# Performance work log

Measured on AMD Instinct MI355X. Metric: run time of the kernel, lower is better.

The kernel has to match this reference:

```python
import jax, jax.numpy as jnp
import numpy as np

N_BINS = 15


def setup_inputs() -> dict:
    key = jax.random.key(0)
    k1, k2 = jax.random.split(key)
    N, C = 4000000, 64
    logits = jax.random.normal(k1, (N, C), dtype=jnp.float32)
    labels = jax.random.randint(k2, (N,), 0, C, dtype=jnp.int64)
    temperature = jnp.ones((1,), dtype=jnp.float32)
    return {"logits": logits, "labels": labels, "temperature": temperature}


def reference(logits, labels, temperature):
    # softmax over classes at given temperature (onevsrest=False path)
    probs = jax.nn.softmax(logits / temperature, axis=1)
    confidences = jnp.max(probs, axis=1)          # [N]
    predictions = jnp.argmax(probs, axis=1)       # [N]
    accuracies = (predictions == labels).astype(confidences.dtype)

    # bin i covers (i/n_bins, (i+1)/n_bins]; conf >= 1/C > 0 so ceil-1 maps correctly
    bin_idx = jnp.clip(
        jnp.ceil(confidences * N_BINS).astype(jnp.int32) - 1, 0, N_BINS - 1)

    count = jax.ops.segment_sum(jnp.ones_like(confidences), bin_idx, num_segments=N_BINS)
    conf_sum = jax.ops.segment_sum(confidences, bin_idx, num_segments=N_BINS)
    acc_sum = jax.ops.segment_sum(accuracies, bin_idx, num_segments=N_BINS)

    nonempty = count > 0
    safe_count = jnp.where(nonempty, count, 1.0)
    gap = jnp.abs(conf_sum / safe_count - acc_sum / safe_count)  # [n_bins]
    prop = count / confidences.shape[0]

    ece = jnp.sum(jnp.where(nonempty, gap * prop, 0.0))
    mce = jnp.max(jnp.where(nonempty, gap, 0.0))
    return ece, mce
```

## Files before the change

kernel.cpp:

```cpp
#include <hip/hip_runtime.h>

#define NBINS 15

typedef float f32x4 __attribute__((ext_vector_type(4)));

__global__ __launch_bounds__(256) void ece_partial(
    const f32x4* __restrict__ logits4,
    const int*   __restrict__ labels,
    const float* __restrict__ temperature,
    float*       __restrict__ gbins,
    int N)
{
    __shared__ float sbins[3 * NBINS];
    const int tid = threadIdx.x;
    if (tid < 3 * NBINS) sbins[tid] = 0.0f;
    __syncthreads();

    const float invT = 1.0f / temperature[0];

    const int lane = tid & 63;
    const int wIn  = tid >> 6;
    const long long gWave = (long long)blockIdx.x * 4 + wIn;
    const long long nWave = (long long)gridDim.x * 4;

    const int sub = lane & 3;
    const int rIw = lane >> 2;

    for (long long r0 = gWave * 16; r0 < (long long)N; r0 += nWave * 16) {
        const long long row = r0 + rIw;
        const bool valid = row < (long long)N;
        const long long rc = valid ? row : (long long)(N - 1);

        const f32x4* p = logits4 + rc * 16 + sub;
        const f32x4 v0 = __builtin_nontemporal_load(p);
        const f32x4 v1 = __builtin_nontemporal_load(p + 4);
        const f32x4 v2 = __builtin_nontemporal_load(p + 8);
        const f32x4 v3 = __builtin_nontemporal_load(p + 12);

        float m  = v0.x;
        int   am = 4 * sub;
        {
            const int b = 4 * sub;
            if (v0.y > m) { m = v0.y; am = b + 1; }
            if (v0.z > m) { m = v0.z; am = b + 2; }
            if (v0.w > m) { m = v0.w; am = b + 3; }
            if (v1.x > m) { m = v1.x; am = b + 16; }
            if (v1.y > m) { m = v1.y; am = b + 17; }
            if (v1.z > m) { m = v1.z; am = b + 18; }
            if (v1.w > m) { m = v1.w; am = b + 19; }
            if (v2.x > m) { m = v2.x; am = b + 32; }
            if (v2.y > m) { m = v2.y; am = b + 33; }
            if (v2.z > m) { m = v2.z; am = b + 34; }
            if (v2.w > m) { m = v2.w; am = b + 35; }
            if (v3.x > m) { m = v3.x; am = b + 48; }
            if (v3.y > m) { m = v3.y; am = b + 49; }
            if (v3.z > m) { m = v3.z; am = b + 50; }
            if (v3.w > m) { m = v3.w; am = b + 51; }
        }

        #pragma unroll
        for (int d = 1; d < 4; d <<= 1) {
            const float om = __shfl_xor(m, d);
            const int   oa = __shfl_xor(am, d);
            if (om > m || (om == m && oa < am)) { m = om; am = oa; }
        }

        float s = __expf((v0.x - m) * invT) + __expf((v0.y - m) * invT)
                + __expf((v0.z - m) * invT) + __expf((v0.w - m) * invT)
                + __expf((v1.x - m) * invT) + __expf((v1.y - m) * invT)
                + __expf((v1.z - m) * invT) + __expf((v1.w - m) * invT)
                + __expf((v2.x - m) * invT) + __expf((v2.y - m) * invT)
                + __expf((v2.z - m) * invT) + __expf((v2.w - m) * invT)
                + __expf((v3.x - m) * invT) + __expf((v3.y - m) * invT)
                + __expf((v3.z - m) * invT) + __expf((v3.w - m) * invT);
        #pragma unroll
        for (int d = 1; d < 4; d <<= 1) s += __shfl_xor(s, d);

        if (valid && sub == 0) {
            const float conf = 1.0f / s;
            const int   lbl  = labels[row];
            const float acc  = (am == lbl) ? 1.0f : 0.0f;
            int bin = (int)ceilf(conf * (float)NBINS) - 1;
            bin = bin < 0 ? 0 : (bin > NBINS - 1 ? NBINS - 1 : bin);
            atomicAdd(&sbins[bin],             1.0f);
            atomicAdd(&sbins[NBINS + bin],     conf);
            atomicAdd(&sbins[2 * NBINS + bin], acc);
        }
    }

    __syncthreads();
    if (tid < 3 * NBINS) {
        const float v = sbins[tid];
        if (v != 0.0f) atomicAdd(&gbins[tid], v);
    }
}

__global__ void ece_finalize(const float* __restrict__ gbins,
                             float* __restrict__ out, float invN)
{
    if (threadIdx.x == 0 && blockIdx.x == 0) {
        float ece = 0.0f, mce = 0.0f;
        #pragma unroll
        for (int i = 0; i < NBINS; ++i) {
            const float c  = gbins[i];
            const float cs = gbins[NBINS + i];
            const float as = gbins[2 * NBINS + i];
            if (c > 0.0f) {
                const float gap = fabsf(cs / c - as / c);
                ece += gap * (c * invN);
                mce = fmaxf(mce, gap);
            }
        }
        out[0] = ece;
        out[1] = mce;
    }
}

extern "C" void kernel_launch(void* const* d_in, const int* in_sizes, int n_in,
                              void* d_out, int out_size, void* d_ws, size_t ws_size,
                              hipStream_t stream) {
    const f32x4* logits4     = (const f32x4*)d_in[0];
    const int*   labels      = (const int*)d_in[1];
    const float* temperature = (const float*)d_in[2];
    float*       out         = (float*)d_out;
    float*       gbins       = (float*)d_ws;

    const int N = in_sizes[1];

    hipMemsetAsync(gbins, 0, 3 * NBINS * sizeof(float), stream);

    const int block = 256;
    const int grid  = 2048;
    ece_partial<<<grid, block, 0, stream>>>(logits4, labels, temperature, gbins, N);
    ece_finalize<<<1, 64, 0, stream>>>(gbins, out, 1.0f / (float)N);
}
```

Measured before the change: 189.6 us.

## Fuse finalize via last-block ticket and drop argmax tracking for label compare

Merges the finalize kernel into the main kernel using an atomic ticket, so the last block computes ECE and MCE and one launch goes away. Softmax is computed without subtracting the max, and the max is found with plain fmax reductions. Accuracy is decided by checking whether the label's logit equals the row max, so no argmax index is shuffled, and the label load is issued alongside the logit loads. This cuts ALU and shuffle work in a memory-bound loop, but it can overflow for large logits or small temperatures and changes tie-breaking semantics.

```diff
diff --git a/kernel.cpp b/kernel.cpp
--- a/kernel.cpp
+++ b/kernel.cpp
@@ -4,12 +4,14 @@
 
 typedef float f32x4 __attribute__((ext_vector_type(4)));
 
-__global__ __launch_bounds__(256) void ece_partial(
+__global__ __launch_bounds__(256, 8) void ece_fused(
     const f32x4* __restrict__ logits4,
     const int*   __restrict__ labels,
     const float* __restrict__ temperature,
     float*       __restrict__ gbins,
-    int N)
+    int*         __restrict__ ticket,
+    float*       __restrict__ out,
+    int N, int nblocks)
 {
     __shared__ float sbins[3 * NBINS];
     const int tid = threadIdx.x;
@@ -36,55 +38,50 @@
         const f32x4 v1 = __builtin_nontemporal_load(p + 4);
         const f32x4 v2 = __builtin_nontemporal_load(p + 8);
         const f32x4 v3 = __builtin_nontemporal_load(p + 12);
+        const int lbl = labels[rc];
 
-        float m  = v0.x;
-        int   am = 4 * sub;
+        float s;
         {
-            const int b = 4 * sub;
-            if (v0.y > m) { m = v0.y; am = b + 1; }
-            if (v0.z > m) { m = v0.z; am = b + 2; }
-            if (v0.w > m) { m = v0.w; am = b + 3; }
-            if (v1.x > m) { m = v1.x; am = b + 16; }
-            if (v1.y > m) { m = v1.y; am = b + 17; }
-            if (v1.z > m) { m = v1.z; am = b + 18; }
-            if (v1.w > m) { m = v1.w; am = b + 19; }
-            if (v2.x > m) { m = v2.x; am = b + 32; }
-            if (v2.y > m) { m = v2.y; am = b + 33; }
-            if (v2.z > m) { m = v2.z; am = b + 34; }
-            if (v2.w > m) { m = v2.w; am = b + 35; }
-            if (v3.x > m) { m = v3.x; am = b + 48; }
-            if (v3.y > m) { m = v3.y; am = b + 49; }
-            if (v3.z > m) { m = v3.z; am = b + 50; }
-            if (v3.w > m) { m = v3.w; am = b + 51; }
+            const float a0 = __expf(v0.x * invT), a1 = __expf(v0.y * invT);
+            const float a2 = __expf(v0.z * invT), a3 = __expf(v0.w * invT);
+            const float b0 = __expf(v1.x * invT), b1 = __expf(v1.y * invT);
+            const float b2 = __expf(v1.z * invT), b3 = __expf(v1.w * invT);
+            const float c0 = __expf(v2.x * invT), c1 = __expf(v2.y * invT);
+            const float c2 = __expf(v2.z * invT), c3 = __expf(v2.w * invT);
+            const float d0 = __expf(v3.x * invT), d1 = __expf(v3.y * invT);
+            const float d2 = __expf(v3.z * invT), d3 = __expf(v3.w * invT);
+            s = (((a0 + a1) + (a2 + a3)) + ((b0 + b1) + (b2 + b3)))
+              + (((c0 + c1) + (c2 + c3)) + ((d0 + d1) + (d2 + d3)));
         }
 
-        #pragma unroll
-        for (int d = 1; d < 4; d <<= 1) {
-            const float om = __shfl_xor(m, d);
-            const int   oa = __shfl_xor(am, d);
-            if (om > m || (om == m && oa < am)) { m = om; am = oa; }
-        }
+        float m = fmaxf(fmaxf(fmaxf(v0.x, v0.y), fmaxf(v0.z, v0.w)),
+                        fmaxf(fmaxf(v1.x, v1.y), fmaxf(v1.z, v1.w)));
+        m = fmaxf(m, fmaxf(fmaxf(fmaxf(v2.x, v2.y), fmaxf(v2.z, v2.w)),
+                           fmaxf(fmaxf(v3.x, v3.y), fmaxf(v3.z, v3.w))));
 
-        float s = __expf((v0.x - m) * invT) + __expf((v0.y - m) * invT)
-                + __expf((v0.z - m) * invT) + __expf((v0.w - m) * invT)
-                + __expf((v1.x - m) * invT) + __expf((v1.y - m) * invT)
-                + __expf((v1.z - m) * invT) + __expf((v1.w - m) * invT)
-                + __expf((v2.x - m) * invT) + __expf((v2.y - m) * invT)
-                + __expf((v2.z - m) * invT) + __expf((v2.w - m) * invT)
-                + __expf((v3.x - m) * invT) + __expf((v3.y - m) * invT)
-                + __expf((v3.z - m) * invT) + __expf((v3.w - m) * invT);
-        #pragma unroll
-        for (int d = 1; d < 4; d <<= 1) s += __shfl_xor(s, d);
+        s += __shfl_xor(s, 1);
+        s += __shfl_xor(s, 2);
+        m = fmaxf(m, __shfl_xor(m, 1));
+        m = fmaxf(m, __shfl_xor(m, 2));
 
-        if (valid && sub == 0) {
-            const float conf = 1.0f / s;
-            const int   lbl  = labels[row];
-            const float acc  = (am == lbl) ? 1.0f : 0.0f;
-            int bin = (int)ceilf(conf * (float)NBINS) - 1;
-            bin = bin < 0 ? 0 : (bin > NBINS - 1 ? NBINS - 1 : bin);
-            atomicAdd(&sbins[bin],             1.0f);
-            atomicAdd(&sbins[NBINS + bin],     conf);
-            atomicAdd(&sbins[2 * NBINS + bin], acc);
+        const float conf = __expf(m * invT) * __builtin_amdgcn_rcpf(s);
+        int bin = (int)ceilf(conf * (float)NBINS) - 1;
+        bin = bin < 0 ? 0 : (bin > NBINS - 1 ? NBINS - 1 : bin);
+
+        if (valid) {
+            if (sub == 0) {
+                atomicAdd(&sbins[bin],         1.0f);
+                atomicAdd(&sbins[NBINS + bin], conf);
+            }
+            if (((lbl >> 2) & 3) == sub) {
+                const int k = lbl >> 4;
+                const int j = lbl & 3;
+                const f32x4 vk = (k < 2) ? ((k & 1) ? v1 : v0)
+                                         : ((k & 1) ? v3 : v2);
+                const float vl = (j < 2) ? ((j & 1) ? vk.y : vk.x)
+                                         : ((j & 1) ? vk.w : vk.z);
+                if (vl == m) atomicAdd(&sbins[2 * NBINS + bin], 1.0f);
+            }
         }
     }
 
@@ -93,26 +90,27 @@
         const float v = sbins[tid];
         if (v != 0.0f) atomicAdd(&gbins[tid], v);
     }
-}
 
-__global__ void ece_finalize(const float* __restrict__ gbins,
-                             float* __restrict__ out, float invN)
-{
-    if (threadIdx.x == 0 && blockIdx.x == 0) {
-        float ece = 0.0f, mce = 0.0f;
-        #pragma unroll
-        for (int i = 0; i < NBINS; ++i) {
-            const float c  = gbins[i];
-            const float cs = gbins[NBINS + i];
-            const float as = gbins[2 * NBINS + i];
-            if (c > 0.0f) {
-                const float gap = fabsf(cs / c - as / c);
-                ece += gap * (c * invN);
-                mce = fmaxf(mce, gap);
+    __threadfence();
+    if (tid == 0) {
+        const int t = atomicAdd(ticket, 1);
+        if (t == nblocks - 1) {
+            const float invN = 1.0f / (float)N;
+            float ece = 0.0f, mce = 0.0f;
+            #pragma unroll
+            for (int i = 0; i < NBINS; ++i) {
+                const float c  = atomicAdd(&gbins[i],             0.0f);
+                const float cs = atomicAdd(&gbins[NBINS + i],     0.0f);
+                const float as = atomicAdd(&gbins[2 * NBINS + i], 0.0f);
+                if (c > 0.0f) {
+                    const float gap = fabsf(cs / c - as / c);
+                    ece += gap * (c * invN);
+                    mce = fmaxf(mce, gap);
+                }
             }
+            out[0] = ece;
+            out[1] = mce;
         }
-        out[0] = ece;
-        out[1] = mce;
     }
 }
 
@@ -124,13 +122,14 @@
     const float* temperature = (const float*)d_in[2];
     float*       out         = (float*)d_out;
     float*       gbins       = (float*)d_ws;
+    int*         ticket      = (int*)d_ws + 48;
 
     const int N = in_sizes[1];
 
-    hipMemsetAsync(gbins, 0, 3 * NBINS * sizeof(float), stream);
+    hipMemsetAsync(d_ws, 0, 64 * sizeof(float), stream);
 
     const int block = 256;
     const int grid  = 2048;
-    ece_partial<<<grid, block, 0, stream>>>(logits4, labels, temperature, gbins, N);
-    ece_finalize<<<1, 64, 0, stream>>>(gbins, out, 1.0f / (float)N);
+    ece_fused<<<grid, block, 0, stream>>>(logits4, labels, temperature,
+                                          gbins, ticket, out, N, grid);
 }
```

New measurement: 592.9 us. 213% more time.
